# Kernel optimization log

Measured on AMD Instinct MI355X. Metric: run time of the kernel, lower is better.

The kernel has to match this reference:

```python
import jax, jax.numpy as jnp
import numpy as np

T, D, I, E, K = 256, 2048, 5632, 8, 2
P = (I * D + 4) // 5  # TQ1_0: 5 ternary values per byte
_MULT = (1, 3, 9, 27, 81)


def _unpack_tq10(packed, out_dim, in_dim):
    # packed: int32 [P], each value is a base-3 byte encoding 5 ternary digits
    digits = jnp.stack([(packed // m) % 3 for m in _MULT], axis=1)  # [P,5]
    w = digits.reshape(-1)[: out_dim * in_dim] - 1  # {-1,0,+1}
    return w.reshape(out_dim, in_dim).astype(jnp.float32)


def _tmm(x, w_packed, s, out_dim, in_dim):
    # ternary_matmul_direct: dequant ternary weight, per-output-row scale
    w = _unpack_tq10(w_packed, out_dim, in_dim)  # [out,in]
    return (x @ w.T) * s.reshape(1, -1)


def setup_inputs() -> dict:
    key = jax.random.key(0)
    ks = jax.random.split(key, 16)
    inp = {}
    inp["x"] = jax.random.normal(ks[0], (T, D), jnp.float32)
    inp["router_w"] = jax.random.normal(ks[1], (E, D), jnp.float32) * 0.02
    inp["gate_packed"] = jax.random.randint(ks[2], (E, P), 0, 243, jnp.int32)
    inp["up_packed"] = jax.random.randint(ks[3], (E, P), 0, 243, jnp.int32)
    inp["down_packed"] = jax.random.randint(ks[4], (E, P), 0, 243, jnp.int32)
    inp["gate_s"] = jax.random.uniform(ks[5], (E, I, 1), jnp.float32, 0.01, 0.05)
    inp["up_s"] = jax.random.uniform(ks[6], (E, I, 1), jnp.float32, 0.01, 0.05)
    inp["down_s"] = jax.random.uniform(ks[7], (E, D, 1), jnp.float32, 0.01, 0.05)
    inp["sh_gate_w"] = jax.random.randint(ks[8], (I, D), -127, 128, jnp.int32)
    inp["sh_up_w"] = jax.random.randint(ks[9], (I, D), -127, 128, jnp.int32)
    inp["sh_down_w"] = jax.random.randint(ks[10], (D, I), -127, 128, jnp.int32)
    inp["sh_gate_s"] = jax.random.uniform(ks[11], (I, 1), jnp.float32, 0.005, 0.02)
    inp["sh_up_s"] = jax.random.uniform(ks[12], (I, 1), jnp.float32, 0.005, 0.02)
    inp["sh_down_s"] = jax.random.uniform(ks[13], (D, 1), jnp.float32, 0.005, 0.02)
    return inp


def reference(x, router_w, gate_packed, up_packed, down_packed,
              gate_s, up_s, down_s,
              sh_gate_w, sh_up_w, sh_down_w,
              sh_gate_s, sh_up_s, sh_down_s):
    n_tok = x.shape[0]
    # ---- router: top-k + softmax over selected logits -> dense gate matrix [T,E]
    logits = x @ router_w.T
    topv, topi = jax.lax.top_k(logits, K)
    probs = jax.nn.softmax(topv, axis=-1)
    gates = jnp.zeros((n_tok, E), x.dtype).at[jnp.arange(n_tok)[:, None], topi].add(probs)
    # ---- shared INT8 SwiGLU expert (dequant matmul, per-row fp scale)
    g = jax.nn.silu((x @ sh_gate_w.T.astype(jnp.float32)) * sh_gate_s.reshape(1, -1))
    u = (x @ sh_up_w.T.astype(jnp.float32)) * sh_up_s.reshape(1, -1)
    out = ((g * u) @ sh_down_w.T.astype(jnp.float32)) * sh_down_s.reshape(1, -1)
    # ---- routed ternary TQ1_0 experts (unpack -> dequant -> SwiGLU)
    for e in range(E):
        ge = jax.nn.silu(_tmm(x, gate_packed[e], gate_s[e], I, D))
        ue = _tmm(x, up_packed[e], up_s[e], I, D)
        ye = _tmm(ge * ue, down_packed[e], down_s[e], D, I)
        out = out + gates[:, e:e + 1] * ye
    return out
```

## Files before the change

### kernel.cpp

```cpp
#include <hip/hip_runtime.h>
#include <hip/hip_bf16.h>
#include <stdint.h>

#define TT 256
#define DD 2048
#define II 5632
#define EE 8
#define PP 2306868

typedef __attribute__((ext_vector_type(8))) short bf16x8;
typedef __attribute__((ext_vector_type(4))) float f32x4;

__device__ __forceinline__ ushort f2b_rne(float f) {
  __hip_bfloat16 h = __float2bfloat16(f);
  return __builtin_bit_cast(ushort, h);
}
__device__ __forceinline__ ushort f2b_exact(float f) {
  return (ushort)(__builtin_bit_cast(uint32_t, f) >> 16);
}

__global__ __launch_bounds__(64) void k_router(const float* __restrict__ x,
                                               const float* __restrict__ rw,
                                               int* __restrict__ cnt,
                                               int* __restrict__ tok,
                                               float* __restrict__ tokg) {
  const int t = blockIdx.x;
  const int lane = threadIdx.x;
  const float* xp = x + t * DD;
  float lg[EE];
#pragma unroll
  for (int e = 0; e < EE; ++e) {
    const float* wp = rw + e * DD;
    float acc = 0.f;
    for (int d = lane; d < DD; d += 64) acc += xp[d] * wp[d];
#pragma unroll
    for (int off = 32; off > 0; off >>= 1) acc += __shfl_down(acc, off, 64);
    lg[e] = acc;
  }
  if (lane == 0) {
    int e1 = 0; float v1 = lg[0];
#pragma unroll
    for (int e = 1; e < EE; ++e) if (lg[e] > v1) { v1 = lg[e]; e1 = e; }
    int e2 = -1; float v2 = -3.4e38f;
#pragma unroll
    for (int e = 0; e < EE; ++e) if (e != e1 && lg[e] > v2) { v2 = lg[e]; e2 = e; }
    float ex2 = __expf(v2 - v1);
    float inv = 1.f / (1.f + ex2);
    int s1 = atomicAdd(&cnt[e1], 1);
    tok[e1 * TT + s1] = t; tokg[e1 * TT + s1] = inv;
    int s2 = atomicAdd(&cnt[e2], 1);
    tok[e2 * TT + s2] = t; tokg[e2 * TT + s2] = ex2 * inv;
  }
}

__global__ __launch_bounds__(256) void k_xcast(const float* __restrict__ x,
                                               ushort* __restrict__ xb) {
  int i = (blockIdx.x * 256 + threadIdx.x) * 8;
  float4 a = *(const float4*)(x + i);
  float4 b = *(const float4*)(x + i + 4);
  ushort o[8];
  o[0] = f2b_rne(a.x); o[1] = f2b_rne(a.y); o[2] = f2b_rne(a.z); o[3] = f2b_rne(a.w);
  o[4] = f2b_rne(b.x); o[5] = f2b_rne(b.y); o[6] = f2b_rne(b.z); o[7] = f2b_rne(b.w);
  *(uint4*)(xb + i) = *(uint4*)&o[0];
}

__device__ __forceinline__ void stage_a(const ushort* __restrict__ src, int ld,
                                        const int* rows, int k0,
                                        ushort (*A)[72], int tid) {
#pragma unroll
  for (int it = 0; it < 2; ++it) {
    int slot = tid + it * 256;
    int r = slot >> 3, cg = slot & 7;
    int rg = rows[r];
    uint4 v = make_uint4(0u, 0u, 0u, 0u);
    if (rg >= 0) v = *(const uint4*)(src + (long)rg * ld + k0 + cg * 8);
    *(uint4*)&A[r][cg * 8] = v;
  }
}

__device__ __forceinline__ void stage_tern(const int* __restrict__ packed,
                                           int n0, int k0, int din,
                                           ushort (*B)[72], int tid) {
#pragma unroll
  for (int it = 0; it < 2; ++it) {
    int slot = tid + it * 256;
    int r = slot >> 3, j = slot & 7;
    int q = (n0 + r) * din + k0;
    int a = (int)((unsigned)q / 5u);
    int bend = (int)(((unsigned)q + 63u) / 5u);
    int pidx = a + 2 * j;
    int c0 = pidx * 5 - q;
    uint32_t p0 = (pidx     <= bend) ? (uint32_t)packed[pidx]     : 0u;
    uint32_t p1 = (pidx + 1 <= bend) ? (uint32_t)packed[pidx + 1] : 0u;
#pragma unroll
    for (int i = 0; i < 5; ++i) {
      uint32_t q0 = (p0 * 171u) >> 9; uint32_t d0 = p0 - q0 * 3u;
      uint32_t q1 = (p1 * 171u) >> 9; uint32_t d1 = p1 - q1 * 3u;
      ushort w0 = (d0 == 0u) ? (ushort)0xBF80 : ((d0 == 2u) ? (ushort)0x3F80 : (ushort)0);
      ushort w1 = (d1 == 0u) ? (ushort)0xBF80 : ((d1 == 2u) ? (ushort)0x3F80 : (ushort)0);
      int c = c0 + i;
      if ((unsigned)c < 64u) B[r][c] = w0;
      if ((unsigned)(c + 5) < 64u) B[r][c + 5] = w1;
      p0 = q0; p1 = q1;
    }
  }
}

__device__ __forceinline__ void stage_i8(const int* __restrict__ w,
                                         int n0, int k0, int din,
                                         ushort (*B)[72], int tid) {
  int r = tid >> 2, cg = tid & 3;
  const int4* p = (const int4*)(w + (long)(n0 + r) * din + k0 + cg * 16);
  ushort tmp[16];
#pragma unroll
  for (int v4 = 0; v4 < 4; ++v4) {
    int4 v = p[v4];
    tmp[v4 * 4 + 0] = f2b_exact((float)v.x);
    tmp[v4 * 4 + 1] = f2b_exact((float)v.y);
    tmp[v4 * 4 + 2] = f2b_exact((float)v.z);
    tmp[v4 * 4 + 3] = f2b_exact((float)v.w);
  }
  *(uint4*)&B[r][cg * 16]     = *(uint4*)&tmp[0];
  *(uint4*)&B[r][cg * 16 + 8] = *(uint4*)&tmp[8];
}

__global__ __launch_bounds__(256) void k_sh_gateup(const ushort* __restrict__ xb,
                                                   const int* __restrict__ wg,
                                                   const int* __restrict__ wu,
                                                   const float* __restrict__ sg_,
                                                   const float* __restrict__ su_,
                                                   ushort* __restrict__ hsh) {
  const int n0 = blockIdx.x * 64;
  const int m0 = blockIdx.y * 64;
  const int tid = threadIdx.x;
  __shared__ ushort A[64][72];
  __shared__ ushort Bg[64][72];
  __shared__ ushort Bu[64][72];
  __shared__ int rows[64];
  if (tid < 64) rows[tid] = m0 + tid;
  f32x4 accg[4], accu[4];
#pragma unroll
  for (int m = 0; m < 4; ++m) { accg[m] = {0.f,0.f,0.f,0.f}; accu[m] = {0.f,0.f,0.f,0.f}; }
  const int lane = tid & 63, wid = tid >> 6;
  const int col = lane & 15, kg = lane >> 4;
  for (int kt = 0; kt < DD / 64; ++kt) {
    int k0 = kt * 64;
    __syncthreads();
    stage_a(xb, DD, rows, k0, A, tid);
    stage_i8(wg, n0, k0, DD, Bg, tid);
    stage_i8(wu, n0, k0, DD, Bu, tid);
    __syncthreads();
#pragma unroll
    for (int kh = 0; kh < 2; ++kh) {
      int kc = kh * 32 + kg * 8;
      bf16x8 bg = *(const bf16x8*)&Bg[wid * 16 + col][kc];
      bf16x8 bu = *(const bf16x8*)&Bu[wid * 16 + col][kc];
#pragma unroll
      for (int m = 0; m < 4; ++m) {
        bf16x8 av = *(const bf16x8*)&A[m * 16 + col][kc];
        accg[m] = __builtin_amdgcn_mfma_f32_16x16x32_bf16(av, bg, accg[m], 0, 0, 0);
        accu[m] = __builtin_amdgcn_mfma_f32_16x16x32_bf16(av, bu, accu[m], 0, 0, 0);
      }
    }
  }
  const int n_abs = n0 + wid * 16 + col;
  const float sg = sg_[n_abs];
  const float su = su_[n_abs];
#pragma unroll
  for (int m = 0; m < 4; ++m) {
#pragma unroll
    for (int i = 0; i < 4; ++i) {
      int mr = m * 16 + kg * 4 + i;
      float g = accg[m][i] * sg;
      float u = accu[m][i] * su;
      float h = g / (1.f + __expf(-g)) * u;
      hsh[(long)(m0 + mr) * II + n_abs] = f2b_rne(h);
    }
  }
}

__global__ __launch_bounds__(256) void k_sh_down(const ushort* __restrict__ hsh,
                                                 const int* __restrict__ wd,
                                                 const float* __restrict__ sd_,
                                                 float* __restrict__ out) {
  const int n0 = blockIdx.x * 64;
  const int m0 = blockIdx.y * 64;
  const int tid = threadIdx.x;
  __shared__ ushort A[64][72];
  __shared__ ushort B[64][72];
  __shared__ int rows[64];
  if (tid < 64) rows[tid] = m0 + tid;
  f32x4 acc[4];
#pragma unroll
  for (int m = 0; m < 4; ++m) acc[m] = {0.f,0.f,0.f,0.f};
  const int lane = tid & 63, wid = tid >> 6;
  const int col = lane & 15, kg = lane >> 4;
  for (int kt = 0; kt < II / 64; ++kt) {
    int k0 = kt * 64;
    __syncthreads();
    stage_a(hsh, II, rows, k0, A, tid);
    stage_i8(wd, n0, k0, II, B, tid);
    __syncthreads();
#pragma unroll
    for (int kh = 0; kh < 2; ++kh) {
      int kc = kh * 32 + kg * 8;
      bf16x8 bv = *(const bf16x8*)&B[wid * 16 + col][kc];
#pragma unroll
      for (int m = 0; m < 4; ++m) {
        bf16x8 av = *(const bf16x8*)&A[m * 16 + col][kc];
        acc[m] = __builtin_amdgcn_mfma_f32_16x16x32_bf16(av, bv, acc[m], 0, 0, 0);
      }
    }
  }
  const int n_abs = n0 + wid * 16 + col;
  const float sd = sd_[n_abs];
#pragma unroll
  for (int m = 0; m < 4; ++m) {
#pragma unroll
    for (int i = 0; i < 4; ++i) {
      int mr = m * 16 + kg * 4 + i;
      out[(long)(m0 + mr) * DD + n_abs] = acc[m][i] * sd;
    }
  }
}

__global__ __launch_bounds__(256) void k_moe_gateup(const ushort* __restrict__ xb,
                                                    const int* __restrict__ gate_p,
                                                    const int* __restrict__ up_p,
                                                    const float* __restrict__ gate_s,
                                                    const float* __restrict__ up_s,
                                                    const int* __restrict__ cnt,
                                                    const int* __restrict__ tok,
                                                    ushort* __restrict__ hrt) {
  const int e = blockIdx.z;
  const int ne = cnt[e];
  const int m0 = blockIdx.y * 64;
  if (m0 >= ne) return;
  const int n0 = blockIdx.x * 64;
  const int tid = threadIdx.x;
  __shared__ ushort A[64][72];
  __shared__ ushort Bg[64][72];
  __shared__ ushort Bu[64][72];
  __shared__ int rows[64];
  if (tid < 64) {
    int s = m0 + tid;
    rows[tid] = (s < ne) ? tok[e * TT + s] : -1;
  }
  const int* gp = gate_p + (long)e * PP;
  const int* up = up_p + (long)e * PP;
  f32x4 accg[4], accu[4];
#pragma unroll
  for (int m = 0; m < 4; ++m) { accg[m] = {0.f,0.f,0.f,0.f}; accu[m] = {0.f,0.f,0.f,0.f}; }
  const int lane = tid & 63, wid = tid >> 6;
  const int col = lane & 15, kg = lane >> 4;
  for (int kt = 0; kt < DD / 64; ++kt) {
    int k0 = kt * 64;
    __syncthreads();
    stage_a(xb, DD, rows, k0, A, tid);
    stage_tern(gp, n0, k0, DD, Bg, tid);
    stage_tern(up, n0, k0, DD, Bu, tid);
    __syncthreads();
#pragma unroll
    for (int kh = 0; kh < 2; ++kh) {
      int kc = kh * 32 + kg * 8;
      bf16x8 bg = *(const bf16x8*)&Bg[wid * 16 + col][kc];
      bf16x8 bu = *(const bf16x8*)&Bu[wid * 16 + col][kc];
#pragma unroll
      for (int m = 0; m < 4; ++m) {
        bf16x8 av = *(const bf16x8*)&A[m * 16 + col][kc];
        accg[m] = __builtin_amdgcn_mfma_f32_16x16x32_bf16(av, bg, accg[m], 0, 0, 0);
        accu[m] = __builtin_amdgcn_mfma_f32_16x16x32_bf16(av, bu, accu[m], 0, 0, 0);
      }
    }
  }
  const int n_abs = n0 + wid * 16 + col;
  const float sg = gate_s[(long)e * II + n_abs];
  const float su = up_s[(long)e * II + n_abs];
  ushort* hb = hrt + (long)e * TT * II;
#pragma unroll
  for (int m = 0; m < 4; ++m) {
#pragma unroll
    for (int i = 0; i < 4; ++i) {
      int mr = m * 16 + kg * 4 + i;
      float g = accg[m][i] * sg;
      float u = accu[m][i] * su;
      float h = g / (1.f + __expf(-g)) * u;
      hb[(long)(m0 + mr) * II + n_abs] = f2b_rne(h);
    }
  }
}

__global__ __launch_bounds__(256) void k_moe_down(const ushort* __restrict__ hrt,
                                                  const int* __restrict__ down_p,
                                                  const float* __restrict__ down_s,
                                                  const int* __restrict__ cnt,
                                                  const int* __restrict__ tok,
                                                  const float* __restrict__ tokg,
                                                  float* __restrict__ out) {
  const int e = blockIdx.z;
  const int ne = cnt[e];
  const int m0 = blockIdx.y * 64;
  if (m0 >= ne) return;
  const int n0 = blockIdx.x * 64;
  const int tid = threadIdx.x;
  __shared__ ushort A[64][72];
  __shared__ ushort B[64][72];
  __shared__ int rows[64];
  __shared__ int trow[64];
  __shared__ float tg[64];
  if (tid < 64) {
    int s = m0 + tid;
    int valid = (s < ne);
    rows[tid] = valid ? (e * TT + s) : -1;
    trow[tid] = valid ? tok[e * TT + s] : 0;
    tg[tid]   = valid ? tokg[e * TT + s] : 0.f;
  }
  const int* dp = down_p + (long)e * PP;
  f32x4 acc[4];
#pragma unroll
  for (int m = 0; m < 4; ++m) acc[m] = {0.f,0.f,0.f,0.f};
  const int lane = tid & 63, wid = tid >> 6;
  const int col = lane & 15, kg = lane >> 4;
  for (int kt = 0; kt < II / 64; ++kt) {
    int k0 = kt * 64;
    __syncthreads();
    stage_a(hrt, II, rows, k0, A, tid);
    stage_tern(dp, n0, k0, II, B, tid);
    __syncthreads();
#pragma unroll
    for (int kh = 0; kh < 2; ++kh) {
      int kc = kh * 32 + kg * 8;
      bf16x8 bv = *(const bf16x8*)&B[wid * 16 + col][kc];
#pragma unroll
      for (int m = 0; m < 4; ++m) {
        bf16x8 av = *(const bf16x8*)&A[m * 16 + col][kc];
        acc[m] = __builtin_amdgcn_mfma_f32_16x16x32_bf16(av, bv, acc[m], 0, 0, 0);
      }
    }
  }
  const int n_abs = n0 + wid * 16 + col;
  const float sd = down_s[(long)e * DD + n_abs];
#pragma unroll
  for (int m = 0; m < 4; ++m) {
#pragma unroll
    for (int i = 0; i < 4; ++i) {
      int mr = m * 16 + kg * 4 + i;
      if (m0 + mr < ne) {
        float v = acc[m][i] * sd * tg[mr];
        atomicAdd(&out[(long)trow[mr] * DD + n_abs], v);
      }
    }
  }
}

extern "C" void kernel_launch(void* const* d_in, const int* in_sizes, int n_in,
                              void* d_out, int out_size, void* d_ws, size_t ws_size,
                              hipStream_t stream) {
  const float* x        = (const float*)d_in[0];
  const float* router_w = (const float*)d_in[1];
  const int*   gate_p   = (const int*)d_in[2];
  const int*   up_p     = (const int*)d_in[3];
  const int*   down_p   = (const int*)d_in[4];
  const float* gate_s   = (const float*)d_in[5];
  const float* up_s     = (const float*)d_in[6];
  const float* down_s   = (const float*)d_in[7];
  const int*   shg      = (const int*)d_in[8];
  const int*   shu      = (const int*)d_in[9];
  const int*   shd      = (const int*)d_in[10];
  const float* shg_s    = (const float*)d_in[11];
  const float* shu_s    = (const float*)d_in[12];
  const float* shd_s    = (const float*)d_in[13];
  float* out = (float*)d_out;

  char* ws = (char*)d_ws;
  int*    cnt  = (int*)ws;
  int*    tok  = (int*)(ws + 1024);
  float*  tokg = (float*)(ws + 1024 + 8192);
  ushort* xb   = (ushort*)(ws + 32768);
  ushort* hsh  = (ushort*)(ws + 32768 + 1048576);
  ushort* hrt  = (ushort*)(ws + 32768 + 1048576 + 2883584);

  hipMemsetAsync(cnt, 0, 64, stream);
  k_router<<<TT, 64, 0, stream>>>(x, router_w, cnt, tok, tokg);
  k_xcast<<<(TT * DD) / (256 * 8), 256, 0, stream>>>(x, xb);
  k_sh_gateup<<<dim3(II / 64, TT / 64), 256, 0, stream>>>(xb, shg, shu, shg_s, shu_s, hsh);
  k_sh_down<<<dim3(DD / 64, TT / 64), 256, 0, stream>>>(hsh, shd, shd_s, out);
  k_moe_gateup<<<dim3(II / 64, TT / 64, EE), 256, 0, stream>>>(xb, gate_p, up_p, gate_s, up_s,
                                                               cnt, tok, hrt);
  k_moe_down<<<dim3(DD / 64, TT / 64, EE), 256, 0, stream>>>(hrt, down_p, down_s,
                                                             cnt, tok, tokg, out);
}
```

Baseline: 1.018 ms.

## Merge shared and routed experts into fused LDS-free kernels with split-K down projection

The kernel set is rebuilt. The bf16 cast of x moves into the router kernel. The shared and routed gate/up GEMMs are merged into one launch selected by blockIdx.z, and likewise the down GEMMs. The new kernels drop LDS staging and instead build MFMA fragments straight from global memory, using a new ternary decoder that combines three packed bytes and extracts digits with v_cvt_pk_bf16_f32. The down projections are split over K with atomic accumulation into an output zeroed by memset. This removes launches, syncthreads and LDS traffic and improves occupancy, but the A and B loads are no longer shared across waves through LDS, and there are more atomics.

```diff
diff --git a/kernel.cpp b/kernel.cpp
--- a/kernel.cpp
+++ b/kernel.cpp
@@ -10,23 +10,70 @@
 
 typedef __attribute__((ext_vector_type(8))) short bf16x8;
 typedef __attribute__((ext_vector_type(4))) float f32x4;
+typedef unsigned int uint;
 
 __device__ __forceinline__ ushort f2b_rne(float f) {
   __hip_bfloat16 h = __float2bfloat16(f);
   return __builtin_bit_cast(ushort, h);
 }
-__device__ __forceinline__ ushort f2b_exact(float f) {
-  return (ushort)(__builtin_bit_cast(uint32_t, f) >> 16);
+
+__device__ __forceinline__ uint pk_bf16(float lo, float hi) {
+  uint r;
+  asm("v_cvt_pk_bf16_f32 %0, %1, %2" : "=v"(r) : "v"(lo), "v"(hi));
+  return r;
+}
+
+__device__ __forceinline__ bf16x8 ld_a(const ushort* p) {
+  uint4 v = *(const uint4*)p;
+  return __builtin_bit_cast(bf16x8, v);
+}
+
+__device__ __forceinline__ bf16x8 tern_frag(const int* __restrict__ pk, uint i0, uint ph) {
+  uint p0 = (uint)pk[i0], p1 = (uint)pk[i0 + 1], p2 = (uint)pk[i0 + 2];
+  uint P = p0 + 243u * p1 + 59049u * p2;
+  uint c1 = P / 3u, c2 = c1 / 3u, c3 = c2 / 3u, c4 = c3 / 3u;
+  uint Q = ph == 0 ? P : (ph == 1 ? c1 : (ph == 2 ? c2 : (ph == 3 ? c3 : c4)));
+  uint w0, w1, w2, w3;
+#define DIGPAIR(wout) { uint qa = Q / 3u; float flo = (float)(int)(Q - 3u * qa) - 1.0f; \
+    uint qb = qa / 3u; float fhi = (float)(int)(qa - 3u * qb) - 1.0f; Q = qb;          \
+    wout = pk_bf16(flo, fhi); }
+  DIGPAIR(w0) DIGPAIR(w1) DIGPAIR(w2) DIGPAIR(w3)
+#undef DIGPAIR
+  uint4 u = make_uint4(w0, w1, w2, w3);
+  return __builtin_bit_cast(bf16x8, u);
+}
+
+__device__ __forceinline__ bf16x8 i8_frag(const int* __restrict__ w, long off) {
+  int4 a = *(const int4*)(w + off);
+  int4 b = *(const int4*)(w + off + 4);
+  uint4 u;
+  u.x = pk_bf16((float)a.x, (float)a.y);
+  u.y = pk_bf16((float)a.z, (float)a.w);
+  u.z = pk_bf16((float)b.x, (float)b.y);
+  u.w = pk_bf16((float)b.z, (float)b.w);
+  return __builtin_bit_cast(bf16x8, u);
 }
 
 __global__ __launch_bounds__(64) void k_router(const float* __restrict__ x,
                                                const float* __restrict__ rw,
                                                int* __restrict__ cnt,
                                                int* __restrict__ tok,
-                                               float* __restrict__ tokg) {
+                                               float* __restrict__ tokg,
+                                               ushort* __restrict__ xb) {
   const int t = blockIdx.x;
   const int lane = threadIdx.x;
-  const float* xp = x + t * DD;
+  const float* xp = x + (long)t * DD;
+  ushort* xbp = xb + (long)t * DD;
+#pragma unroll
+  for (int it = 0; it < DD / (64 * 8); ++it) {
+    int d = lane * 8 + it * 512;
+    float4 a = *(const float4*)(xp + d);
+    float4 b = *(const float4*)(xp + d + 4);
+    ushort o[8];
+    o[0] = f2b_rne(a.x); o[1] = f2b_rne(a.y); o[2] = f2b_rne(a.z); o[3] = f2b_rne(a.w);
+    o[4] = f2b_rne(b.x); o[5] = f2b_rne(b.y); o[6] = f2b_rne(b.z); o[7] = f2b_rne(b.w);
+    *(uint4*)(xbp + d) = *(uint4*)&o[0];
+  }
   float lg[EE];
 #pragma unroll
   for (int e = 0; e < EE; ++e) {
@@ -53,303 +100,194 @@
   }
 }
 
-__global__ __launch_bounds__(256) void k_xcast(const float* __restrict__ x,
-                                               ushort* __restrict__ xb) {
-  int i = (blockIdx.x * 256 + threadIdx.x) * 8;
-  float4 a = *(const float4*)(x + i);
-  float4 b = *(const float4*)(x + i + 4);
-  ushort o[8];
-  o[0] = f2b_rne(a.x); o[1] = f2b_rne(a.y); o[2] = f2b_rne(a.z); o[3] = f2b_rne(a.w);
-  o[4] = f2b_rne(b.x); o[5] = f2b_rne(b.y); o[6] = f2b_rne(b.z); o[7] = f2b_rne(b.w);
-  *(uint4*)(xb + i) = *(uint4*)&o[0];
-}
-
-__device__ __forceinline__ void stage_a(const ushort* __restrict__ src, int ld,
-                                        const int* rows, int k0,
-                                        ushort (*A)[72], int tid) {
-#pragma unroll
-  for (int it = 0; it < 2; ++it) {
-    int slot = tid + it * 256;
-    int r = slot >> 3, cg = slot & 7;
-    int rg = rows[r];
-    uint4 v = make_uint4(0u, 0u, 0u, 0u);
-    if (rg >= 0) v = *(const uint4*)(src + (long)rg * ld + k0 + cg * 8);
-    *(uint4*)&A[r][cg * 8] = v;
-  }
-}
-
-__device__ __forceinline__ void stage_tern(const int* __restrict__ packed,
-                                           int n0, int k0, int din,
-                                           ushort (*B)[72], int tid) {
-#pragma unroll
-  for (int it = 0; it < 2; ++it) {
-    int slot = tid + it * 256;
-    int r = slot >> 3, j = slot & 7;
-    int q = (n0 + r) * din + k0;
-    int a = (int)((unsigned)q / 5u);
-    int bend = (int)(((unsigned)q + 63u) / 5u);
-    int pidx = a + 2 * j;
-    int c0 = pidx * 5 - q;
-    uint32_t p0 = (pidx     <= bend) ? (uint32_t)packed[pidx]     : 0u;
-    uint32_t p1 = (pidx + 1 <= bend) ? (uint32_t)packed[pidx + 1] : 0u;
-#pragma unroll
-    for (int i = 0; i < 5; ++i) {
-      uint32_t q0 = (p0 * 171u) >> 9; uint32_t d0 = p0 - q0 * 3u;
-      uint32_t q1 = (p1 * 171u) >> 9; uint32_t d1 = p1 - q1 * 3u;
-      ushort w0 = (d0 == 0u) ? (ushort)0xBF80 : ((d0 == 2u) ? (ushort)0x3F80 : (ushort)0);
-      ushort w1 = (d1 == 0u) ? (ushort)0xBF80 : ((d1 == 2u) ? (ushort)0x3F80 : (ushort)0);
-      int c = c0 + i;
-      if ((unsigned)c < 64u) B[r][c] = w0;
-      if ((unsigned)(c + 5) < 64u) B[r][c + 5] = w1;
-      p0 = q0; p1 = q1;
-    }
-  }
-}
-
-__device__ __forceinline__ void stage_i8(const int* __restrict__ w,
-                                         int n0, int k0, int din,
-                                         ushort (*B)[72], int tid) {
-  int r = tid >> 2, cg = tid & 3;
-  const int4* p = (const int4*)(w + (long)(n0 + r) * din + k0 + cg * 16);
-  ushort tmp[16];
-#pragma unroll
-  for (int v4 = 0; v4 < 4; ++v4) {
-    int4 v = p[v4];
-    tmp[v4 * 4 + 0] = f2b_exact((float)v.x);
-    tmp[v4 * 4 + 1] = f2b_exact((float)v.y);
-    tmp[v4 * 4 + 2] = f2b_exact((float)v.z);
-    tmp[v4 * 4 + 3] = f2b_exact((float)v.w);
-  }
-  *(uint4*)&B[r][cg * 16]     = *(uint4*)&tmp[0];
-  *(uint4*)&B[r][cg * 16 + 8] = *(uint4*)&tmp[8];
-}
-
-__global__ __launch_bounds__(256) void k_sh_gateup(const ushort* __restrict__ xb,
-                                                   const int* __restrict__ wg,
-                                                   const int* __restrict__ wu,
-                                                   const float* __restrict__ sg_,
-                                                   const float* __restrict__ su_,
-                                                   ushort* __restrict__ hsh) {
-  const int n0 = blockIdx.x * 64;
-  const int m0 = blockIdx.y * 64;
-  const int tid = threadIdx.x;
-  __shared__ ushort A[64][72];
-  __shared__ ushort Bg[64][72];
-  __shared__ ushort Bu[64][72];
-  __shared__ int rows[64];
-  if (tid < 64) rows[tid] = m0 + tid;
-  f32x4 accg[4], accu[4];
-#pragma unroll
-  for (int m = 0; m < 4; ++m) { accg[m] = {0.f,0.f,0.f,0.f}; accu[m] = {0.f,0.f,0.f,0.f}; }
-  const int lane = tid & 63, wid = tid >> 6;
-  const int col = lane & 15, kg = lane >> 4;
-  for (int kt = 0; kt < DD / 64; ++kt) {
-    int k0 = kt * 64;
-    __syncthreads();
-    stage_a(xb, DD, rows, k0, A, tid);
-    stage_i8(wg, n0, k0, DD, Bg, tid);
-    stage_i8(wu, n0, k0, DD, Bu, tid);
-    __syncthreads();
-#pragma unroll
-    for (int kh = 0; kh < 2; ++kh) {
-      int kc = kh * 32 + kg * 8;
-      bf16x8 bg = *(const bf16x8*)&Bg[wid * 16 + col][kc];
-      bf16x8 bu = *(const bf16x8*)&Bu[wid * 16 + col][kc];
-#pragma unroll
-      for (int m = 0; m < 4; ++m) {
-        bf16x8 av = *(const bf16x8*)&A[m * 16 + col][kc];
-        accg[m] = __builtin_amdgcn_mfma_f32_16x16x32_bf16(av, bg, accg[m], 0, 0, 0);
-        accu[m] = __builtin_amdgcn_mfma_f32_16x16x32_bf16(av, bu, accu[m], 0, 0, 0);
-      }
-    }
-  }
-  const int n_abs = n0 + wid * 16 + col;
-  const float sg = sg_[n_abs];
-  const float su = su_[n_abs];
-#pragma unroll
-  for (int m = 0; m < 4; ++m) {
-#pragma unroll
-    for (int i = 0; i < 4; ++i) {
-      int mr = m * 16 + kg * 4 + i;
-      float g = accg[m][i] * sg;
-      float u = accu[m][i] * su;
-      float h = g / (1.f + __expf(-g)) * u;
-      hsh[(long)(m0 + mr) * II + n_abs] = f2b_rne(h);
-    }
-  }
-}
-
-__global__ __launch_bounds__(256) void k_sh_down(const ushort* __restrict__ hsh,
-                                                 const int* __restrict__ wd,
-                                                 const float* __restrict__ sd_,
-                                                 float* __restrict__ out) {
-  const int n0 = blockIdx.x * 64;
-  const int m0 = blockIdx.y * 64;
-  const int tid = threadIdx.x;
-  __shared__ ushort A[64][72];
-  __shared__ ushort B[64][72];
-  __shared__ int rows[64];
-  if (tid < 64) rows[tid] = m0 + tid;
-  f32x4 acc[4];
-#pragma unroll
-  for (int m = 0; m < 4; ++m) acc[m] = {0.f,0.f,0.f,0.f};
-  const int lane = tid & 63, wid = tid >> 6;
-  const int col = lane & 15, kg = lane >> 4;
-  for (int kt = 0; kt < II / 64; ++kt) {
-    int k0 = kt * 64;
-    __syncthreads();
-    stage_a(hsh, II, rows, k0, A, tid);
-    stage_i8(wd, n0, k0, II, B, tid);
-    __syncthreads();
-#pragma unroll
-    for (int kh = 0; kh < 2; ++kh) {
-      int kc = kh * 32 + kg * 8;
-      bf16x8 bv = *(const bf16x8*)&B[wid * 16 + col][kc];
-#pragma unroll
-      for (int m = 0; m < 4; ++m) {
-        bf16x8 av = *(const bf16x8*)&A[m * 16 + col][kc];
-        acc[m] = __builtin_amdgcn_mfma_f32_16x16x32_bf16(av, bv, acc[m], 0, 0, 0);
-      }
-    }
-  }
-  const int n_abs = n0 + wid * 16 + col;
-  const float sd = sd_[n_abs];
-#pragma unroll
-  for (int m = 0; m < 4; ++m) {
-#pragma unroll
-    for (int i = 0; i < 4; ++i) {
-      int mr = m * 16 + kg * 4 + i;
-      out[(long)(m0 + mr) * DD + n_abs] = acc[m][i] * sd;
-    }
-  }
-}
-
-__global__ __launch_bounds__(256) void k_moe_gateup(const ushort* __restrict__ xb,
+__global__ __launch_bounds__(256) void k_gateup_all(const ushort* __restrict__ xb,
+                                                    const int* __restrict__ cnt,
+                                                    const int* __restrict__ tok,
                                                     const int* __restrict__ gate_p,
                                                     const int* __restrict__ up_p,
                                                     const float* __restrict__ gate_s,
                                                     const float* __restrict__ up_s,
-                                                    const int* __restrict__ cnt,
-                                                    const int* __restrict__ tok,
+                                                    const int* __restrict__ shg,
+                                                    const int* __restrict__ shu,
+                                                    const float* __restrict__ shg_s,
+                                                    const float* __restrict__ shu_s,
+                                                    ushort* __restrict__ hsh,
                                                     ushort* __restrict__ hrt) {
-  const int e = blockIdx.z;
-  const int ne = cnt[e];
-  const int m0 = blockIdx.y * 64;
-  if (m0 >= ne) return;
   const int n0 = blockIdx.x * 64;
   const int tid = threadIdx.x;
-  __shared__ ushort A[64][72];
-  __shared__ ushort Bg[64][72];
-  __shared__ ushort Bu[64][72];
-  __shared__ int rows[64];
-  if (tid < 64) {
-    int s = m0 + tid;
-    rows[tid] = (s < ne) ? tok[e * TT + s] : -1;
-  }
-  const int* gp = gate_p + (long)e * PP;
-  const int* up = up_p + (long)e * PP;
-  f32x4 accg[4], accu[4];
-#pragma unroll
-  for (int m = 0; m < 4; ++m) { accg[m] = {0.f,0.f,0.f,0.f}; accu[m] = {0.f,0.f,0.f,0.f}; }
   const int lane = tid & 63, wid = tid >> 6;
-  const int col = lane & 15, kg = lane >> 4;
-  for (int kt = 0; kt < DD / 64; ++kt) {
-    int k0 = kt * 64;
-    __syncthreads();
-    stage_a(xb, DD, rows, k0, A, tid);
-    stage_tern(gp, n0, k0, DD, Bg, tid);
-    stage_tern(up, n0, k0, DD, Bu, tid);
-    __syncthreads();
-#pragma unroll
-    for (int kh = 0; kh < 2; ++kh) {
-      int kc = kh * 32 + kg * 8;
-      bf16x8 bg = *(const bf16x8*)&Bg[wid * 16 + col][kc];
-      bf16x8 bu = *(const bf16x8*)&Bu[wid * 16 + col][kc];
-#pragma unroll
-      for (int m = 0; m < 4; ++m) {
-        bf16x8 av = *(const bf16x8*)&A[m * 16 + col][kc];
-        accg[m] = __builtin_amdgcn_mfma_f32_16x16x32_bf16(av, bg, accg[m], 0, 0, 0);
-        accu[m] = __builtin_amdgcn_mfma_f32_16x16x32_bf16(av, bu, accu[m], 0, 0, 0);
-      }
-    }
-  }
-  const int n_abs = n0 + wid * 16 + col;
-  const float sg = gate_s[(long)e * II + n_abs];
-  const float su = up_s[(long)e * II + n_abs];
-  ushort* hb = hrt + (long)e * TT * II;
-#pragma unroll
-  for (int m = 0; m < 4; ++m) {
-#pragma unroll
-    for (int i = 0; i < 4; ++i) {
-      int mr = m * 16 + kg * 4 + i;
-      float g = accg[m][i] * sg;
-      float u = accu[m][i] * su;
-      float h = g / (1.f + __expf(-g)) * u;
-      hb[(long)(m0 + mr) * II + n_abs] = f2b_rne(h);
-    }
-  }
-}
-
-__global__ __launch_bounds__(256) void k_moe_down(const ushort* __restrict__ hrt,
+  const int col = lane & 15, kg8 = (lane >> 4) * 8;
+  const int n_lane = n0 + wid * 16 + col;
+  const int z = blockIdx.z;
+
+  if (z == 8) {
+    if (blockIdx.y >= 2) return;
+    const int m0 = blockIdx.y * 128;
+    const long nd = (long)n_lane * DD;
+    f32x4 ag[8], au[8];
+#pragma unroll
+    for (int m = 0; m < 8; ++m) { ag[m] = {0.f,0.f,0.f,0.f}; au[m] = {0.f,0.f,0.f,0.f}; }
+#pragma unroll 1
+    for (int kt = 0; kt < DD / 64; ++kt) {
+#pragma unroll
+      for (int kh = 0; kh < 2; ++kh) {
+        const int kf = kt * 64 + kh * 32 + kg8;
+        bf16x8 bg = i8_frag(shg, nd + kf);
+        bf16x8 bu = i8_frag(shu, nd + kf);
+#pragma unroll
+        for (int m = 0; m < 8; ++m) {
+          bf16x8 av = ld_a(xb + (long)(m0 + m * 16 + col) * DD + kf);
+          ag[m] = __builtin_amdgcn_mfma_f32_16x16x32_bf16(av, bg, ag[m], 0, 0, 0);
+          au[m] = __builtin_amdgcn_mfma_f32_16x16x32_bf16(av, bu, au[m], 0, 0, 0);
+        }
+      }
+    }
+    const float sg = shg_s[n_lane];
+    const float su = shu_s[n_lane];
+#pragma unroll
+    for (int m = 0; m < 8; ++m)
+#pragma unroll
+      for (int i = 0; i < 4; ++i) {
+        int mr = m0 + m * 16 + (lane >> 4) * 4 + i;
+        float g = ag[m][i] * sg, u = au[m][i] * su;
+        float h = g / (1.f + __expf(-g)) * u;
+        hsh[(long)mr * II + n_lane] = f2b_rne(h);
+      }
+  } else {
+    const int e = z;
+    const int ne = cnt[e];
+    const int m0 = blockIdx.y * 64;
+    if (m0 >= ne) return;
+    long arow[4];
+#pragma unroll
+    for (int m = 0; m < 4; ++m) {
+      int s = m0 + m * 16 + col;
+      if (s >= ne) s = ne - 1;
+      arow[m] = (long)tok[e * TT + s] * DD;
+    }
+    const int* gp = gate_p + (long)e * PP;
+    const int* up = up_p + (long)e * PP;
+    const uint nd = (uint)n_lane * DD;
+    f32x4 ag[4], au[4];
+#pragma unroll
+    for (int m = 0; m < 4; ++m) { ag[m] = {0.f,0.f,0.f,0.f}; au[m] = {0.f,0.f,0.f,0.f}; }
+#pragma unroll 1
+    for (int kt = 0; kt < DD / 64; ++kt) {
+#pragma unroll
+      for (int kh = 0; kh < 2; ++kh) {
+        const int kf = kt * 64 + kh * 32 + kg8;
+        const uint q = nd + (uint)kf;
+        const uint i0 = q / 5u;
+        const uint ph = q - 5u * i0;
+        bf16x8 bg = tern_frag(gp, i0, ph);
+        bf16x8 bu = tern_frag(up, i0, ph);
+#pragma unroll
+        for (int m = 0; m < 4; ++m) {
+          bf16x8 av = ld_a(xb + arow[m] + kf);
+          ag[m] = __builtin_amdgcn_mfma_f32_16x16x32_bf16(av, bg, ag[m], 0, 0, 0);
+          au[m] = __builtin_amdgcn_mfma_f32_16x16x32_bf16(av, bu, au[m], 0, 0, 0);
+        }
+      }
+    }
+    const float sg = gate_s[(long)e * II + n_lane];
+    const float su = up_s[(long)e * II + n_lane];
+    ushort* hb = hrt + (long)e * TT * II;
+#pragma unroll
+    for (int m = 0; m < 4; ++m)
+#pragma unroll
+      for (int i = 0; i < 4; ++i) {
+        int mr = m0 + m * 16 + (lane >> 4) * 4 + i;
+        float g = ag[m][i] * sg, u = au[m][i] * su;
+        float h = g / (1.f + __expf(-g)) * u;
+        hb[(long)mr * II + n_lane] = f2b_rne(h);
+      }
+  }
+}
+
+__global__ __launch_bounds__(256) void k_down_all(const ushort* __restrict__ hsh,
+                                                  const ushort* __restrict__ hrt,
                                                   const int* __restrict__ down_p,
                                                   const float* __restrict__ down_s,
+                                                  const int* __restrict__ shd,
+                                                  const float* __restrict__ shd_s,
                                                   const int* __restrict__ cnt,
                                                   const int* __restrict__ tok,
                                                   const float* __restrict__ tokg,
                                                   float* __restrict__ out) {
-  const int e = blockIdx.z;
-  const int ne = cnt[e];
-  const int m0 = blockIdx.y * 64;
-  if (m0 >= ne) return;
   const int n0 = blockIdx.x * 64;
   const int tid = threadIdx.x;
-  __shared__ ushort A[64][72];
-  __shared__ ushort B[64][72];
-  __shared__ int rows[64];
-  __shared__ int trow[64];
-  __shared__ float tg[64];
-  if (tid < 64) {
-    int s = m0 + tid;
-    int valid = (s < ne);
-    rows[tid] = valid ? (e * TT + s) : -1;
-    trow[tid] = valid ? tok[e * TT + s] : 0;
-    tg[tid]   = valid ? tokg[e * TT + s] : 0.f;
-  }
-  const int* dp = down_p + (long)e * PP;
-  f32x4 acc[4];
-#pragma unroll
-  for (int m = 0; m < 4; ++m) acc[m] = {0.f,0.f,0.f,0.f};
   const int lane = tid & 63, wid = tid >> 6;
-  const int col = lane & 15, kg = lane >> 4;
-  for (int kt = 0; kt < II / 64; ++kt) {
-    int k0 = kt * 64;
-    __syncthreads();
-    stage_a(hrt, II, rows, k0, A, tid);
-    stage_tern(dp, n0, k0, II, B, tid);
-    __syncthreads();
-#pragma unroll
-    for (int kh = 0; kh < 2; ++kh) {
-      int kc = kh * 32 + kg * 8;
-      bf16x8 bv = *(const bf16x8*)&B[wid * 16 + col][kc];
-#pragma unroll
-      for (int m = 0; m < 4; ++m) {
-        bf16x8 av = *(const bf16x8*)&A[m * 16 + col][kc];
-        acc[m] = __builtin_amdgcn_mfma_f32_16x16x32_bf16(av, bv, acc[m], 0, 0, 0);
-      }
-    }
-  }
-  const int n_abs = n0 + wid * 16 + col;
-  const float sd = down_s[(long)e * DD + n_abs];
-#pragma unroll
-  for (int m = 0; m < 4; ++m) {
-#pragma unroll
-    for (int i = 0; i < 4; ++i) {
-      int mr = m * 16 + kg * 4 + i;
-      if (m0 + mr < ne) {
-        float v = acc[m][i] * sd * tg[mr];
-        atomicAdd(&out[(long)trow[mr] * DD + n_abs], v);
-      }
-    }
+  const int col = lane & 15, kg8 = (lane >> 4) * 8;
+  const int n_lane = n0 + wid * 16 + col;
+  const int z = blockIdx.z;
+
+  if (z >= 16) {
+    if (blockIdx.y >= 2) return;
+    const int ks = z - 16;
+    const int m0 = blockIdx.y * 128;
+    const long nd = (long)n_lane * II;
+    f32x4 acc[8];
+#pragma unroll
+    for (int m = 0; m < 8; ++m) acc[m] = {0.f,0.f,0.f,0.f};
+#pragma unroll 1
+    for (int kt = ks * 22; kt < ks * 22 + 22; ++kt) {
+#pragma unroll
+      for (int kh = 0; kh < 2; ++kh) {
+        const int kf = kt * 64 + kh * 32 + kg8;
+        bf16x8 bv = i8_frag(shd, nd + kf);
+#pragma unroll
+        for (int m = 0; m < 8; ++m) {
+          bf16x8 av = ld_a(hsh + (long)(m0 + m * 16 + col) * II + kf);
+          acc[m] = __builtin_amdgcn_mfma_f32_16x16x32_bf16(av, bv, acc[m], 0, 0, 0);
+        }
+      }
+    }
+    const float sd = shd_s[n_lane];
+#pragma unroll
+    for (int m = 0; m < 8; ++m)
+#pragma unroll
+      for (int i = 0; i < 4; ++i) {
+        int mr = m0 + m * 16 + (lane >> 4) * 4 + i;
+        atomicAdd(&out[(long)mr * DD + n_lane], acc[m][i] * sd);
+      }
+  } else {
+    const int e = z >> 1, ks = z & 1;
+    const int ne = cnt[e];
+    const int m0 = blockIdx.y * 64;
+    if (m0 >= ne) return;
+    const int* dp = down_p + (long)e * PP;
+    const ushort* abase = hrt + (long)(e * TT + m0 + col) * II;
+    const uint nd = (uint)n_lane * II;
+    f32x4 acc[4];
+#pragma unroll
+    for (int m = 0; m < 4; ++m) acc[m] = {0.f,0.f,0.f,0.f};
+#pragma unroll 1
+    for (int kt = ks * 44; kt < ks * 44 + 44; ++kt) {
+#pragma unroll
+      for (int kh = 0; kh < 2; ++kh) {
+        const int kf = kt * 64 + kh * 32 + kg8;
+        const uint q = nd + (uint)kf;
+        const uint i0 = q / 5u;
+        const uint ph = q - 5u * i0;
+        bf16x8 bv = tern_frag(dp, i0, ph);
+#pragma unroll
+        for (int m = 0; m < 4; ++m) {
+          bf16x8 av = ld_a(abase + (long)m * 16 * II + kf);
+          acc[m] = __builtin_amdgcn_mfma_f32_16x16x32_bf16(av, bv, acc[m], 0, 0, 0);
+        }
+      }
+    }
+    const float sd = down_s[(long)e * DD + n_lane];
+#pragma unroll
+    for (int m = 0; m < 4; ++m)
+#pragma unroll
+      for (int i = 0; i < 4; ++i) {
+        int mr = m0 + m * 16 + (lane >> 4) * 4 + i;
+        if (mr < ne) {
+          float v = acc[m][i] * sd * tokg[e * TT + mr];
+          atomicAdd(&out[(long)tok[e * TT + mr] * DD + n_lane], v);
+        }
+      }
   }
 }
 
@@ -375,18 +313,16 @@
   char* ws = (char*)d_ws;
   int*    cnt  = (int*)ws;
   int*    tok  = (int*)(ws + 1024);
-  float*  tokg = (float*)(ws + 1024 + 8192);
+  float*  tokg = (float*)(ws + 9216);
   ushort* xb   = (ushort*)(ws + 32768);
   ushort* hsh  = (ushort*)(ws + 32768 + 1048576);
   ushort* hrt  = (ushort*)(ws + 32768 + 1048576 + 2883584);
 
   hipMemsetAsync(cnt, 0, 64, stream);
-  k_router<<<TT, 64, 0, stream>>>(x, router_w, cnt, tok, tokg);
-  k_xcast<<<(TT * DD) / (256 * 8), 256, 0, stream>>>(x, xb);
-  k_sh_gateup<<<dim3(II / 64, TT / 64), 256, 0, stream>>>(xb, shg, shu, shg_s, shu_s, hsh);
-  k_sh_down<<<dim3(DD / 64, TT / 64), 256, 0, stream>>>(hsh, shd, shd_s, out);
-  k_moe_gateup<<<dim3(II / 64, TT / 64, EE), 256, 0, stream>>>(xb, gate_p, up_p, gate_s, up_s,
-                                                               cnt, tok, hrt);
-  k_moe_down<<<dim3(DD / 64, TT / 64, EE), 256, 0, stream>>>(hrt, down_p, down_s,
-                                                             cnt, tok, tokg, out);
-}
+  hipMemsetAsync(out, 0, (size_t)TT * DD * 4, stream);
+  k_router<<<TT, 64, 0, stream>>>(x, router_w, cnt, tok, tokg, xb);
+  k_gateup_all<<<dim3(88, 4, 9), 256, 0, stream>>>(xb, cnt, tok, gate_p, up_p, gate_s, up_s,
+                                                   shg, shu, shg_s, shu_s, hsh, hrt);
+  k_down_all<<<dim3(32, 4, 20), 256, 0, stream>>>(hsh, hrt, down_p, down_s, shd, shd_s,
+                                                  cnt, tok, tokg, out);
+}
```

Result: no change. 1.000 ms (-1.7%).
